# Optimization experiments

Hardware: AMD Instinct MI355X
Metric: run time of the kernel (lower is better)

Reference implementation:

```python
import jax, jax.numpy as jnp
import numpy as np

B, S, D, K = 16384, 32, 64, 3
LN_EPS = 1e-6
ENT_EPS = 1e-10
SUM_EPS = 1e-6


def _layernorm(x, g, b):
    m = x.mean(-1, keepdims=True)
    v = ((x - m) ** 2).mean(-1, keepdims=True)
    return (x - m) * jax.lax.rsqrt(v + LN_EPS) * g + b


def setup_inputs() -> dict:
    key = jax.random.key(0)
    ks = jax.random.split(key, 8)
    return {
        "gw_r": jax.random.normal(ks[0], (B, D), jnp.float32),
        "gw_i": jax.random.normal(ks[1], (B, D), jnp.float32),
        "mem_r": jax.random.normal(ks[2], (B, S, D), jnp.float32),
        "mem_i": jax.random.normal(ks[3], (B, S, D), jnp.float32),
        # gate_net: Linear(2D -> 1); stored as [in, out]
        "Wg": jax.random.normal(ks[4], (2 * D, 1), jnp.float32) * 0.05,
        "bg": jnp.zeros((1,), jnp.float32),
        # address_net: Linear(2D -> slots)
        "Wa": jax.random.normal(ks[5], (2 * D, S), jnp.float32) * 0.05,
        "ba": jnp.zeros((S,), jnp.float32),
        # StableComplexNorm affine params
        "g_r": jnp.ones((D,), jnp.float32),
        "b_r": jnp.zeros((D,), jnp.float32),
        "g_i": jnp.ones((D,), jnp.float32),
        "b_i": jnp.zeros((D,), jnp.float32),
    }


def reference(gw_r, gw_i, mem_r, mem_i, Wg, bg, Wa, ba, g_r, b_r, g_i, b_i):
    # --- Read: cosine-style similarity Re(conj(mem) * q).sum(-1) ---
    sim = jnp.einsum("bsd,bd->bs", mem_r, gw_r) + jnp.einsum("bsd,bd->bs", mem_i, gw_i)
    sim = sim - jax.lax.stop_gradient(sim.max(-1, keepdims=True))
    attn = jax.nn.softmax(sim, axis=-1)  # [B, S]
    read_r = jnp.einsum("bs,bsd->bd", attn, mem_r)
    read_i = jnp.einsum("bs,bsd->bd", attn, mem_i)

    # --- Write gate + address ---
    flat = jnp.concatenate([gw_r, gw_i], axis=-1)  # [B, 2D]
    write_gate = jax.nn.sigmoid(flat @ Wg + bg)  # [B, 1]
    logits = flat @ Wa + ba  # [B, S]
    logits = logits - jax.lax.stop_gradient(logits.max(-1, keepdims=True))
    ww = jax.nn.softmax(logits, axis=-1)  # [B, S]
    slot_entropy = -(ww * jnp.log(ww + ENT_EPS)).sum(-1).mean()

    # --- Top-k sparse scatter write weights ---
    top_vals, top_idx = jax.lax.top_k(ww, K)  # [B, K]
    sparse = jnp.zeros_like(ww).at[jnp.arange(B)[:, None], top_idx].set(top_vals)
    sparse = sparse / (sparse.sum(-1, keepdims=True) + SUM_EPS)

    # effective_update: [B, S, 1]
    eu = write_gate[:, None, :] * sparse[..., None]
    next_r = (1.0 - eu) * mem_r + eu * gw_r[:, None, :]
    next_i = (1.0 - eu) * mem_i + eu * gw_i[:, None, :]

    # --- Dual LayerNorm on real/imag independently ---
    next_r = _layernorm(next_r, g_r, b_r)
    next_i = _layernorm(next_i, g_i, b_i)

    return (read_r, read_i, next_r, next_i, slot_entropy)
```

## Files before the change

kernel.cpp:

```cpp
#include <hip/hip_runtime.h>
#include <cstddef>

constexpr int Bn = 16384;
constexpr int Sn = 32;
constexpr int Dn = 64;

__device__ __forceinline__ float red16(float v) {
    v += __shfl_xor(v, 1);
    v += __shfl_xor(v, 2);
    v += __shfl_xor(v, 4);
    v += __shfl_xor(v, 8);
    return v;
}

__device__ __forceinline__ float4 red_groups(float4 v) {
    v.x += __shfl_xor(v.x, 16); v.y += __shfl_xor(v.y, 16);
    v.z += __shfl_xor(v.z, 16); v.w += __shfl_xor(v.w, 16);
    v.x += __shfl_xor(v.x, 32); v.y += __shfl_xor(v.y, 32);
    v.z += __shfl_xor(v.z, 32); v.w += __shfl_xor(v.w, 32);
    return v;
}

__global__ __launch_bounds__(256, 4) void amem_fwd(
    const float* __restrict__ gw_r, const float* __restrict__ gw_i,
    const float* __restrict__ mem_r, const float* __restrict__ mem_i,
    const float* __restrict__ Wg,   const float* __restrict__ bg,
    const float* __restrict__ Wa,   const float* __restrict__ ba,
    const float* __restrict__ g_r,  const float* __restrict__ b_r,
    const float* __restrict__ g_i,  const float* __restrict__ b_i,
    float* __restrict__ o_read_r, float* __restrict__ o_read_i,
    float* __restrict__ o_next_r, float* __restrict__ o_next_i,
    float* __restrict__ ws_ent)
{
    __shared__ float sWa[4096];
    __shared__ float lflat[4][128];

    const int tid  = threadIdx.x;
    const int wave = tid >> 6;
    const int l    = tid & 63;
    const int b    = blockIdx.x * 4 + wave;
    const int g    = l >> 4;
    const int q    = l & 15;

    const float4* mr4 = (const float4*)mem_r + (size_t)b * 512;
    const float4* mi4 = (const float4*)mem_i + (size_t)b * 512;
    float4 m_r[8], m_i[8];
#pragma unroll
    for (int k = 0; k < 8; ++k) {
        m_r[k] = mr4[k * 64 + l];
        m_i[k] = mi4[k * 64 + l];
    }
    const float4 q4r = ((const float4*)gw_r)[b * 16 + q];
    const float4 q4i = ((const float4*)gw_i)[b * 16 + q];

    {
        const float4* Wa4 = (const float4*)Wa;
        float4* sWa4 = (float4*)sWa;
#pragma unroll
        for (int j = 0; j < 4; ++j) sWa4[tid + 256 * j] = Wa4[tid + 256 * j];
    }
    if (g == 0)      *(float4*)&lflat[wave][q * 4]      = q4r;
    else if (g == 1) *(float4*)&lflat[wave][64 + q * 4] = q4i;
    __syncthreads();

    float sims[8];
#pragma unroll
    for (int k = 0; k < 8; ++k) {
        float p = m_r[k].x * q4r.x + m_r[k].y * q4r.y + m_r[k].z * q4r.z + m_r[k].w * q4r.w
                + m_i[k].x * q4i.x + m_i[k].y * q4i.y + m_i[k].z * q4i.z + m_i[k].w * q4i.w;
        sims[k] = red16(p);
    }
    float mx = sims[0];
#pragma unroll
    for (int k = 1; k < 8; ++k) mx = fmaxf(mx, sims[k]);
    mx = fmaxf(mx, __shfl_xor(mx, 16));
    mx = fmaxf(mx, __shfl_xor(mx, 32));
    float attn[8];
    float asum = 0.f;
#pragma unroll
    for (int k = 0; k < 8; ++k) { attn[k] = __expf(sims[k] - mx); asum += attn[k]; }
    asum += __shfl_xor(asum, 16);
    asum += __shfl_xor(asum, 32);
    const float ainv = 1.0f / asum;

    float4 rr = {0.f, 0.f, 0.f, 0.f}, ri = {0.f, 0.f, 0.f, 0.f};
#pragma unroll
    for (int k = 0; k < 8; ++k) {
        const float a = attn[k] * ainv;
        rr.x = fmaf(a, m_r[k].x, rr.x); rr.y = fmaf(a, m_r[k].y, rr.y);
        rr.z = fmaf(a, m_r[k].z, rr.z); rr.w = fmaf(a, m_r[k].w, rr.w);
        ri.x = fmaf(a, m_i[k].x, ri.x); ri.y = fmaf(a, m_i[k].y, ri.y);
        ri.z = fmaf(a, m_i[k].z, ri.z); ri.w = fmaf(a, m_i[k].w, ri.w);
    }
    rr = red_groups(rr);
    ri = red_groups(ri);
    if (g == 0) {
        ((float4*)o_read_r)[b * 16 + q] = rr;
        ((float4*)o_read_i)[b * 16 + q] = ri;
    }

    const float4 wg0 = ((const float4*)Wg)[q];
    const float4 wg1 = ((const float4*)Wg)[16 + q];
    float wp = q4r.x * wg0.x + q4r.y * wg0.y + q4r.z * wg0.z + q4r.w * wg0.w
             + q4i.x * wg1.x + q4i.y * wg1.y + q4i.z * wg1.z + q4i.w * wg1.w;
    wp = red16(wp);
    const float wgate = 1.0f / (1.0f + __expf(-(wp + bg[0])));

    const int sl = l & 31;
    const int h  = l >> 5;
    const float* WaL = sWa + h * 2048;
    const float4* lf4 = (const float4*)&lflat[wave][h * 64];
    float a0 = 0.f, a1 = 0.f, a2 = 0.f, a3 = 0.f;
#pragma unroll
    for (int jj = 0; jj < 16; ++jj) {
        const float4 f = lf4[jj];
        const int r0 = jj * 4;
        a0 = fmaf(f.x, WaL[(r0 + 0) * 32 + sl], a0);
        a1 = fmaf(f.y, WaL[(r0 + 1) * 32 + sl], a1);
        a2 = fmaf(f.z, WaL[(r0 + 2) * 32 + sl], a2);
        a3 = fmaf(f.w, WaL[(r0 + 3) * 32 + sl], a3);
    }
    float acc = (a0 + a1) + (a2 + a3);
    acc += __shfl_xor(acc, 32);
    acc += ba[sl];

    float lm = acc;
    lm = fmaxf(lm, __shfl_xor(lm, 1));
    lm = fmaxf(lm, __shfl_xor(lm, 2));
    lm = fmaxf(lm, __shfl_xor(lm, 4));
    lm = fmaxf(lm, __shfl_xor(lm, 8));
    lm = fmaxf(lm, __shfl_xor(lm, 16));
    const float we = __expf(acc - lm);
    float wsum = we;
    wsum += __shfl_xor(wsum, 1);
    wsum += __shfl_xor(wsum, 2);
    wsum += __shfl_xor(wsum, 4);
    wsum += __shfl_xor(wsum, 8);
    wsum += __shfl_xor(wsum, 16);
    const float ww = we / wsum;

    float et = ww * __logf(ww + 1e-10f);
    et += __shfl_xor(et, 1);
    et += __shfl_xor(et, 2);
    et += __shfl_xor(et, 4);
    et += __shfl_xor(et, 8);
    et += __shfl_xor(et, 16);
    if (l == 0) ws_ent[b] = -et;

    float lv = ww;
    float v1, v2, v3;
    int   i1, i2, i3;
#pragma unroll
    for (int pass = 0; pass < 3; ++pass) {
        float bv = lv;
        int   bi = sl;
#pragma unroll
        for (int d = 1; d <= 16; d <<= 1) {
            const float ov = __shfl_xor(bv, d);
            const int   oi = __shfl_xor(bi, d);
            if (ov > bv || (ov == bv && oi < bi)) { bv = ov; bi = oi; }
        }
        if (pass == 0) { v1 = bv; i1 = bi; }
        else if (pass == 1) { v2 = bv; i2 = bi; }
        else { v3 = bv; i3 = bi; }
        if (sl == bi) lv = -1.f;
    }
    const float inv_ssum = 1.0f / (v1 + v2 + v3 + 1e-6f);

    const float4 gr  = ((const float4*)g_r)[q];
    const float4 br  = ((const float4*)b_r)[q];
    const float4 gi  = ((const float4*)g_i)[q];
    const float4 bi4 = ((const float4*)b_i)[q];
    float4* onr = (float4*)o_next_r + (size_t)b * 512;
    float4* oni = (float4*)o_next_i + (size_t)b * 512;

#pragma unroll
    for (int k = 0; k < 8; ++k) {
        const int s = k * 4 + g;
        const float sp = (s == i1) ? v1 : (s == i2) ? v2 : (s == i3) ? v3 : 0.f;
        const float eu = wgate * sp * inv_ssum;
        const float om = 1.f - eu;

        float4 xr, xi;
        xr.x = om * m_r[k].x + eu * q4r.x;
        xr.y = om * m_r[k].y + eu * q4r.y;
        xr.z = om * m_r[k].z + eu * q4r.z;
        xr.w = om * m_r[k].w + eu * q4r.w;
        xi.x = om * m_i[k].x + eu * q4i.x;
        xi.y = om * m_i[k].y + eu * q4i.y;
        xi.z = om * m_i[k].z + eu * q4i.z;
        xi.w = om * m_i[k].w + eu * q4i.w;

        float sr = (xr.x + xr.y) + (xr.z + xr.w);
        float si = (xi.x + xi.y) + (xi.z + xi.w);
        float qr = xr.x * xr.x; qr = fmaf(xr.y, xr.y, qr); qr = fmaf(xr.z, xr.z, qr); qr = fmaf(xr.w, xr.w, qr);
        float qi = xi.x * xi.x; qi = fmaf(xi.y, xi.y, qi); qi = fmaf(xi.z, xi.z, qi); qi = fmaf(xi.w, xi.w, qi);

#pragma unroll
        for (int d2 = 1; d2 <= 8; d2 <<= 1) {
            sr += __shfl_xor(sr, d2);
            si += __shfl_xor(si, d2);
            qr += __shfl_xor(qr, d2);
            qi += __shfl_xor(qi, d2);
        }

        const float mr_ = sr * (1.f / 64.f);
        const float mi_ = si * (1.f / 64.f);
        const float vr  = qr * (1.f / 64.f) - mr_ * mr_;
        const float vi  = qi * (1.f / 64.f) - mi_ * mi_;
        const float ar  = rsqrtf(vr + 1e-6f);
        const float ai  = rsqrtf(vi + 1e-6f);
        const float cr  = -mr_ * ar;
        const float ci  = -mi_ * ai;

        float4 yr, yi;
        yr.x = fmaf(fmaf(xr.x, ar, cr), gr.x, br.x);
        yr.y = fmaf(fmaf(xr.y, ar, cr), gr.y, br.y);
        yr.z = fmaf(fmaf(xr.z, ar, cr), gr.z, br.z);
        yr.w = fmaf(fmaf(xr.w, ar, cr), gr.w, br.w);
        yi.x = fmaf(fmaf(xi.x, ai, ci), gi.x, bi4.x);
        yi.y = fmaf(fmaf(xi.y, ai, ci), gi.y, bi4.y);
        yi.z = fmaf(fmaf(xi.z, ai, ci), gi.z, bi4.z);
        yi.w = fmaf(fmaf(xi.w, ai, ci), gi.w, bi4.w);
        onr[k * 64 + l] = yr;
        oni[k * 64 + l] = yi;
    }
}

__global__ __launch_bounds__(1024) void ent_reduce(const float* __restrict__ ws_ent,
                                                   float* __restrict__ o_ent)
{
    __shared__ float red[1024];
    const int t = threadIdx.x;
    float s = 0.f;
    for (int i = t; i < Bn; i += 1024) s += ws_ent[i];
    red[t] = s;
    __syncthreads();
    for (int st = 512; st > 0; st >>= 1) {
        if (t < st) red[t] += red[t + st];
        __syncthreads();
    }
    if (t == 0) o_ent[0] = red[0] * (1.0f / (float)Bn);
}

extern "C" void kernel_launch(void* const* d_in, const int* in_sizes, int n_in,
                              void* d_out, int out_size, void* d_ws, size_t ws_size,
                              hipStream_t stream)
{
    const float* gw_r  = (const float*)d_in[0];
    const float* gw_i  = (const float*)d_in[1];
    const float* mem_r = (const float*)d_in[2];
    const float* mem_i = (const float*)d_in[3];
    const float* Wg    = (const float*)d_in[4];
    const float* bg    = (const float*)d_in[5];
    const float* Wa    = (const float*)d_in[6];
    const float* ba    = (const float*)d_in[7];
    const float* g_r   = (const float*)d_in[8];
    const float* b_r   = (const float*)d_in[9];
    const float* g_i   = (const float*)d_in[10];
    const float* b_i   = (const float*)d_in[11];

    float* out = (float*)d_out;
    const size_t nBD  = (size_t)Bn * Dn;
    const size_t nBSD = (size_t)Bn * Sn * Dn;
    float* o_read_r = out;
    float* o_read_i = out + nBD;
    float* o_next_r = out + 2 * nBD;
    float* o_next_i = out + 2 * nBD + nBSD;
    float* o_ent    = out + 2 * nBD + 2 * nBSD;

    float* ws_ent = (float*)d_ws;

    amem_fwd<<<Bn / 4, 256, 0, stream>>>(
        gw_r, gw_i, mem_r, mem_i, Wg, bg, Wa, ba, g_r, b_r, g_i, b_i,
        o_read_r, o_read_i, o_next_r, o_next_i, ws_ent);
    ent_reduce<<<1, 1024, 0, stream>>>(ws_ent, o_ent);
}
```

Before: 122.3 us.

## Stream memory rows twice instead of holding them in registers, raise occupancy

The main kernel no longer keeps all 64 floats of mem_r/mem_i per lane in registers across the whole computation. It reads the memory once to compute similarities and softmax. It then re-reads mem_r and mem_i in two separate passes that fuse the attention read-out with the gated update and LayerNorm. Launch bounds are raised from 4 to 8 blocks per SM to exploit the lower register pressure. The cost is a second read of the 64 MB memory tensors, which likely hits L2/MALL only partially and could increase DRAM traffic for this bandwidth-bound kernel.

Result: slower. 319.8 us (+161.6%).

```diff
diff --git a/kernel.cpp b/kernel.cpp
--- a/kernel.cpp
+++ b/kernel.cpp
@@ -21,7 +21,7 @@
     return v;
 }
 
-__global__ __launch_bounds__(256, 4) void amem_fwd(
+__global__ __launch_bounds__(256, 8) void amem_fwd(
     const float* __restrict__ gw_r, const float* __restrict__ gw_i,
     const float* __restrict__ mem_r, const float* __restrict__ mem_i,
     const float* __restrict__ Wg,   const float* __restrict__ bg,
@@ -42,14 +42,6 @@
     const int g    = l >> 4;
     const int q    = l & 15;
 
-    const float4* mr4 = (const float4*)mem_r + (size_t)b * 512;
-    const float4* mi4 = (const float4*)mem_i + (size_t)b * 512;
-    float4 m_r[8], m_i[8];
-#pragma unroll
-    for (int k = 0; k < 8; ++k) {
-        m_r[k] = mr4[k * 64 + l];
-        m_i[k] = mi4[k * 64 + l];
-    }
     const float4 q4r = ((const float4*)gw_r)[b * 16 + q];
     const float4 q4i = ((const float4*)gw_i)[b * 16 + q];
 
@@ -62,42 +54,6 @@
     if (g == 0)      *(float4*)&lflat[wave][q * 4]      = q4r;
     else if (g == 1) *(float4*)&lflat[wave][64 + q * 4] = q4i;
     __syncthreads();
-
-    float sims[8];
-#pragma unroll
-    for (int k = 0; k < 8; ++k) {
-        float p = m_r[k].x * q4r.x + m_r[k].y * q4r.y + m_r[k].z * q4r.z + m_r[k].w * q4r.w
-                + m_i[k].x * q4i.x + m_i[k].y * q4i.y + m_i[k].z * q4i.z + m_i[k].w * q4i.w;
-        sims[k] = red16(p);
-    }
-    float mx = sims[0];
-#pragma unroll
-    for (int k = 1; k < 8; ++k) mx = fmaxf(mx, sims[k]);
-    mx = fmaxf(mx, __shfl_xor(mx, 16));
-    mx = fmaxf(mx, __shfl_xor(mx, 32));
-    float attn[8];
-    float asum = 0.f;
-#pragma unroll
-    for (int k = 0; k < 8; ++k) { attn[k] = __expf(sims[k] - mx); asum += attn[k]; }
-    asum += __shfl_xor(asum, 16);
-    asum += __shfl_xor(asum, 32);
-    const float ainv = 1.0f / asum;
-
-    float4 rr = {0.f, 0.f, 0.f, 0.f}, ri = {0.f, 0.f, 0.f, 0.f};
-#pragma unroll
-    for (int k = 0; k < 8; ++k) {
-        const float a = attn[k] * ainv;
-        rr.x = fmaf(a, m_r[k].x, rr.x); rr.y = fmaf(a, m_r[k].y, rr.y);
-        rr.z = fmaf(a, m_r[k].z, rr.z); rr.w = fmaf(a, m_r[k].w, rr.w);
-        ri.x = fmaf(a, m_i[k].x, ri.x); ri.y = fmaf(a, m_i[k].y, ri.y);
-        ri.z = fmaf(a, m_i[k].z, ri.z); ri.w = fmaf(a, m_i[k].w, ri.w);
-    }
-    rr = red_groups(rr);
-    ri = red_groups(ri);
-    if (g == 0) {
-        ((float4*)o_read_r)[b * 16 + q] = rr;
-        ((float4*)o_read_i)[b * 16 + q] = ri;
-    }
 
     const float4 wg0 = ((const float4*)Wg)[q];
     const float4 wg1 = ((const float4*)Wg)[16 + q];
@@ -167,63 +123,120 @@
     }
     const float inv_ssum = 1.0f / (v1 + v2 + v3 + 1e-6f);
 
-    const float4 gr  = ((const float4*)g_r)[q];
-    const float4 br  = ((const float4*)b_r)[q];
-    const float4 gi  = ((const float4*)g_i)[q];
-    const float4 bi4 = ((const float4*)b_i)[q];
-    float4* onr = (float4*)o_next_r + (size_t)b * 512;
-    float4* oni = (float4*)o_next_i + (size_t)b * 512;
-
+    const float4* mr4 = (const float4*)mem_r + (size_t)b * 512;
+    const float4* mi4 = (const float4*)mem_i + (size_t)b * 512;
+    float sims[8];
 #pragma unroll
     for (int k = 0; k < 8; ++k) {
-        const int s = k * 4 + g;
-        const float sp = (s == i1) ? v1 : (s == i2) ? v2 : (s == i3) ? v3 : 0.f;
-        const float eu = wgate * sp * inv_ssum;
-        const float om = 1.f - eu;
-
-        float4 xr, xi;
-        xr.x = om * m_r[k].x + eu * q4r.x;
-        xr.y = om * m_r[k].y + eu * q4r.y;
-        xr.z = om * m_r[k].z + eu * q4r.z;
-        xr.w = om * m_r[k].w + eu * q4r.w;
-        xi.x = om * m_i[k].x + eu * q4i.x;
-        xi.y = om * m_i[k].y + eu * q4i.y;
-        xi.z = om * m_i[k].z + eu * q4i.z;
-        xi.w = om * m_i[k].w + eu * q4i.w;
-
-        float sr = (xr.x + xr.y) + (xr.z + xr.w);
-        float si = (xi.x + xi.y) + (xi.z + xi.w);
-        float qr = xr.x * xr.x; qr = fmaf(xr.y, xr.y, qr); qr = fmaf(xr.z, xr.z, qr); qr = fmaf(xr.w, xr.w, qr);
-        float qi = xi.x * xi.x; qi = fmaf(xi.y, xi.y, qi); qi = fmaf(xi.z, xi.z, qi); qi = fmaf(xi.w, xi.w, qi);
-
-#pragma unroll
-        for (int d2 = 1; d2 <= 8; d2 <<= 1) {
-            sr += __shfl_xor(sr, d2);
-            si += __shfl_xor(si, d2);
-            qr += __shfl_xor(qr, d2);
-            qi += __shfl_xor(qi, d2);
+        const float4 a = mr4[k * 64 + l];
+        const float4 c = mi4[k * 64 + l];
+        float p = a.x * q4r.x + a.y * q4r.y + a.z * q4r.z + a.w * q4r.w
+                + c.x * q4i.x + c.y * q4i.y + c.z * q4i.z + c.w * q4i.w;
+        sims[k] = red16(p);
+    }
+    float mx = sims[0];
+#pragma unroll
+    for (int k = 1; k < 8; ++k) mx = fmaxf(mx, sims[k]);
+    mx = fmaxf(mx, __shfl_xor(mx, 16));
+    mx = fmaxf(mx, __shfl_xor(mx, 32));
+    float attn[8];
+    float asum = 0.f;
+#pragma unroll
+    for (int k = 0; k < 8; ++k) { attn[k] = __expf(sims[k] - mx); asum += attn[k]; }
+    asum += __shfl_xor(asum, 16);
+    asum += __shfl_xor(asum, 32);
+    const float ainv = 1.0f / asum;
+#pragma unroll
+    for (int k = 0; k < 8; ++k) attn[k] *= ainv;
+
+    {
+        const float4 gr = ((const float4*)g_r)[q];
+        const float4 br = ((const float4*)b_r)[q];
+        float4* onr = (float4*)o_next_r + (size_t)b * 512;
+        float4 rr = {0.f, 0.f, 0.f, 0.f};
+#pragma unroll
+        for (int k = 0; k < 8; ++k) {
+            const float4 m = mr4[k * 64 + l];
+            rr.x = fmaf(attn[k], m.x, rr.x); rr.y = fmaf(attn[k], m.y, rr.y);
+            rr.z = fmaf(attn[k], m.z, rr.z); rr.w = fmaf(attn[k], m.w, rr.w);
+
+            const int s = k * 4 + g;
+            const float sp = (s == i1) ? v1 : (s == i2) ? v2 : (s == i3) ? v3 : 0.f;
+            const float eu = wgate * sp * inv_ssum;
+            const float om = 1.f - eu;
+
+            float4 x;
+            x.x = om * m.x + eu * q4r.x;
+            x.y = om * m.y + eu * q4r.y;
+            x.z = om * m.z + eu * q4r.z;
+            x.w = om * m.w + eu * q4r.w;
+
+            float sr = (x.x + x.y) + (x.z + x.w);
+            float qr = x.x * x.x; qr = fmaf(x.y, x.y, qr); qr = fmaf(x.z, x.z, qr); qr = fmaf(x.w, x.w, qr);
+#pragma unroll
+            for (int d2 = 1; d2 <= 8; d2 <<= 1) {
+                sr += __shfl_xor(sr, d2);
+                qr += __shfl_xor(qr, d2);
+            }
+            const float mean = sr * (1.f / 64.f);
+            const float var  = qr * (1.f / 64.f) - mean * mean;
+            const float rs   = rsqrtf(var + 1e-6f);
+            const float c0   = -mean * rs;
+
+            float4 y;
+            y.x = fmaf(fmaf(x.x, rs, c0), gr.x, br.x);
+            y.y = fmaf(fmaf(x.y, rs, c0), gr.y, br.y);
+            y.z = fmaf(fmaf(x.z, rs, c0), gr.z, br.z);
+            y.w = fmaf(fmaf(x.w, rs, c0), gr.w, br.w);
+            onr[k * 64 + l] = y;
         }
-
-        const float mr_ = sr * (1.f / 64.f);
-        const float mi_ = si * (1.f / 64.f);
-        const float vr  = qr * (1.f / 64.f) - mr_ * mr_;
-        const float vi  = qi * (1.f / 64.f) - mi_ * mi_;
-        const float ar  = rsqrtf(vr + 1e-6f);
-        const float ai  = rsqrtf(vi + 1e-6f);
-        const float cr  = -mr_ * ar;
-        const float ci  = -mi_ * ai;
-
-        float4 yr, yi;
-        yr.x = fmaf(fmaf(xr.x, ar, cr), gr.x, br.x);
-        yr.y = fmaf(fmaf(xr.y, ar, cr), gr.y, br.y);
-        yr.z = fmaf(fmaf(xr.z, ar, cr), gr.z, br.z);
-        yr.w = fmaf(fmaf(xr.w, ar, cr), gr.w, br.w);
-        yi.x = fmaf(fmaf(xi.x, ai, ci), gi.x, bi4.x);
-        yi.y = fmaf(fmaf(xi.y, ai, ci), gi.y, bi4.y);
-        yi.z = fmaf(fmaf(xi.z, ai, ci), gi.z, bi4.z);
-        yi.w = fmaf(fmaf(xi.w, ai, ci), gi.w, bi4.w);
-        onr[k * 64 + l] = yr;
-        oni[k * 64 + l] = yi;
+        rr = red_groups(rr);
+        if (g == 0) ((float4*)o_read_r)[b * 16 + q] = rr;
+    }
+
+    {
+        const float4 gi  = ((const float4*)g_i)[q];
+        const float4 bi4 = ((const float4*)b_i)[q];
+        float4* oni = (float4*)o_next_i + (size_t)b * 512;
+        float4 ri = {0.f, 0.f, 0.f, 0.f};
+#pragma unroll
+        for (int k = 0; k < 8; ++k) {
+            const float4 m = mi4[k * 64 + l];
+            ri.x = fmaf(attn[k], m.x, ri.x); ri.y = fmaf(attn[k], m.y, ri.y);
+            ri.z = fmaf(attn[k], m.z, ri.z); ri.w = fmaf(attn[k], m.w, ri.w);
+
+            const int s = k * 4 + g;
+            const float sp = (s == i1) ? v1 : (s == i2) ? v2 : (s == i3) ? v3 : 0.f;
+            const float eu = wgate * sp * inv_ssum;
+            const float om = 1.f - eu;
+
+            float4 x;
+            x.x = om * m.x + eu * q4i.x;
+            x.y = om * m.y + eu * q4i.y;
+            x.z = om * m.z + eu * q4i.z;
+            x.w = om * m.w + eu * q4i.w;
+
+            float si = (x.x + x.y) + (x.z + x.w);
+            float qi = x.x * x.x; qi = fmaf(x.y, x.y, qi); qi = fmaf(x.z, x.z, qi); qi = fmaf(x.w, x.w, qi);
+#pragma unroll
+            for (int d2 = 1; d2 <= 8; d2 <<= 1) {
+                si += __shfl_xor(si, d2);
+                qi += __shfl_xor(qi, d2);
+            }
+            const float mean = si * (1.f / 64.f);
+            const float var  = qi * (1.f / 64.f) - mean * mean;
+            const float rs   = rsqrtf(var + 1e-6f);
+            const float c0   = -mean * rs;
+
+            float4 y;
+            y.x = fmaf(fmaf(x.x, rs, c0), gi.x, bi4.x);
+            y.y = fmaf(fmaf(x.y, rs, c0), gi.y, bi4.y);
+            y.z = fmaf(fmaf(x.z, rs, c0), gi.z, bi4.z);
+            y.w = fmaf(fmaf(x.w, rs, c0), gi.w, bi4.w);
+            oni[k * 64 + l] = y;
+        }
+        ri = red_groups(ri);
+        if (g == 0) ((float4*)o_read_i)[b * 16 + q] = ri;
     }
 }
 
```

## Split write-address computation into separate kernel and use DPP reductions

Applied to the files above, without the earlier changes.

Moves the gate, address softmax, entropy and top-3 selection into a lightweight pre-kernel that writes per-row metadata, so the main memory-bound kernel no longer stages Wa into LDS, synchronises, or runs the address matmul. The main kernel reads the metadata, fuses the read-accumulation into the LayerNorm loop, and replaces 16-lane shuffle reductions with DPP row operations. This adds a kernel launch and a small workspace round trip in exchange for lighter LDS use and fewer instructions in the bandwidth-bound path.

Result: slower. 264.8 us (+116.6%).

```diff
diff --git a/kernel.cpp b/kernel.cpp
--- a/kernel.cpp
+++ b/kernel.cpp
@@ -4,6 +4,25 @@
 constexpr int Bn = 16384;
 constexpr int Sn = 32;
 constexpr int Dn = 64;
+
+__device__ __forceinline__ float dpp_add(float v, const int ctrl) {
+    int t;
+    switch (ctrl) {
+        case 0xB1:  t = __builtin_amdgcn_update_dpp(0, __builtin_bit_cast(int, v), 0xB1, 0xF, 0xF, true); break;
+        case 0x4E:  t = __builtin_amdgcn_update_dpp(0, __builtin_bit_cast(int, v), 0x4E, 0xF, 0xF, true); break;
+        case 0x141: t = __builtin_amdgcn_update_dpp(0, __builtin_bit_cast(int, v), 0x141, 0xF, 0xF, true); break;
+        default:    t = __builtin_amdgcn_update_dpp(0, __builtin_bit_cast(int, v), 0x140, 0xF, 0xF, true); break;
+    }
+    return v + __builtin_bit_cast(float, t);
+}
+
+__device__ __forceinline__ float red16_dpp(float v) {
+    v = dpp_add(v, 0xB1);
+    v = dpp_add(v, 0x4E);
+    v = dpp_add(v, 0x141);
+    v = dpp_add(v, 0x140);
+    return v;
+}
 
 __device__ __forceinline__ float red16(float v) {
     v += __shfl_xor(v, 1);
@@ -13,28 +32,125 @@
     return v;
 }
 
-__device__ __forceinline__ float4 red_groups(float4 v) {
-    v.x += __shfl_xor(v.x, 16); v.y += __shfl_xor(v.y, 16);
-    v.z += __shfl_xor(v.z, 16); v.w += __shfl_xor(v.w, 16);
-    v.x += __shfl_xor(v.x, 32); v.y += __shfl_xor(v.y, 32);
-    v.z += __shfl_xor(v.z, 32); v.w += __shfl_xor(v.w, 32);
-    return v;
-}
-
-__global__ __launch_bounds__(256, 4) void amem_fwd(
+__global__ __launch_bounds__(256, 8) void amem_meta(
     const float* __restrict__ gw_r, const float* __restrict__ gw_i,
-    const float* __restrict__ mem_r, const float* __restrict__ mem_i,
     const float* __restrict__ Wg,   const float* __restrict__ bg,
     const float* __restrict__ Wa,   const float* __restrict__ ba,
-    const float* __restrict__ g_r,  const float* __restrict__ b_r,
-    const float* __restrict__ g_i,  const float* __restrict__ b_i,
-    float* __restrict__ o_read_r, float* __restrict__ o_read_i,
-    float* __restrict__ o_next_r, float* __restrict__ o_next_i,
-    float* __restrict__ ws_ent)
+    float* __restrict__ meta, float* __restrict__ ws_ent)
 {
     __shared__ float sWa[4096];
     __shared__ float lflat[4][128];
 
+    const int tid  = threadIdx.x;
+    const int wave = tid >> 6;
+    const int l    = tid & 63;
+    const int g    = l >> 4;
+    const int q    = l & 15;
+    const int sl   = l & 31;
+    const int h    = l >> 5;
+
+    {
+        const float4* Wa4 = (const float4*)Wa;
+        float4* sWa4 = (float4*)sWa;
+#pragma unroll
+        for (int j = 0; j < 4; ++j) sWa4[tid + 256 * j] = Wa4[tid + 256 * j];
+    }
+    __syncthreads();
+
+    const float bg0 = bg[0];
+    const float ba_sl = ba[sl];
+    const float4 wg0 = ((const float4*)Wg)[q];
+    const float4 wg1 = ((const float4*)Wg)[16 + q];
+
+    for (int r = 0; r < 4; ++r) {
+        const int b = blockIdx.x * 16 + wave * 4 + r;
+        const float4 q4r = ((const float4*)gw_r)[b * 16 + q];
+        const float4 q4i = ((const float4*)gw_i)[b * 16 + q];
+
+        if (g == 0)      *(float4*)&lflat[wave][q * 4]      = q4r;
+        else if (g == 1) *(float4*)&lflat[wave][64 + q * 4] = q4i;
+
+        float wp = q4r.x * wg0.x + q4r.y * wg0.y + q4r.z * wg0.z + q4r.w * wg0.w
+                 + q4i.x * wg1.x + q4i.y * wg1.y + q4i.z * wg1.z + q4i.w * wg1.w;
+        wp = red16(wp);
+        const float wgate = 1.0f / (1.0f + __expf(-(wp + bg0)));
+
+        const float* WaL = sWa + h * 2048;
+        const float4* lf4 = (const float4*)&lflat[wave][h * 64];
+        float a0 = 0.f, a1 = 0.f, a2 = 0.f, a3 = 0.f;
+#pragma unroll
+        for (int jj = 0; jj < 16; ++jj) {
+            const float4 f = lf4[jj];
+            const int r0 = jj * 4;
+            a0 = fmaf(f.x, WaL[(r0 + 0) * 32 + sl], a0);
+            a1 = fmaf(f.y, WaL[(r0 + 1) * 32 + sl], a1);
+            a2 = fmaf(f.z, WaL[(r0 + 2) * 32 + sl], a2);
+            a3 = fmaf(f.w, WaL[(r0 + 3) * 32 + sl], a3);
+        }
+        float acc = (a0 + a1) + (a2 + a3);
+        acc += __shfl_xor(acc, 32);
+        acc += ba_sl;
+
+        float lm = acc;
+        lm = fmaxf(lm, __shfl_xor(lm, 1));
+        lm = fmaxf(lm, __shfl_xor(lm, 2));
+        lm = fmaxf(lm, __shfl_xor(lm, 4));
+        lm = fmaxf(lm, __shfl_xor(lm, 8));
+        lm = fmaxf(lm, __shfl_xor(lm, 16));
+        const float we = __expf(acc - lm);
+        float wsum = we;
+        wsum += __shfl_xor(wsum, 1);
+        wsum += __shfl_xor(wsum, 2);
+        wsum += __shfl_xor(wsum, 4);
+        wsum += __shfl_xor(wsum, 8);
+        wsum += __shfl_xor(wsum, 16);
+        const float ww = we / wsum;
+
+        float et = ww * __logf(ww + 1e-10f);
+        et += __shfl_xor(et, 1);
+        et += __shfl_xor(et, 2);
+        et += __shfl_xor(et, 4);
+        et += __shfl_xor(et, 8);
+        et += __shfl_xor(et, 16);
+
+        float lv = ww;
+        float v1, v2, v3;
+        int   i1, i2, i3;
+#pragma unroll
+        for (int pass = 0; pass < 3; ++pass) {
+            float bv = lv;
+            int   bi = sl;
+#pragma unroll
+            for (int d = 1; d <= 16; d <<= 1) {
+                const float ov = __shfl_xor(bv, d);
+                const int   oi = __shfl_xor(bi, d);
+                if (ov > bv || (ov == bv && oi < bi)) { bv = ov; bi = oi; }
+            }
+            if (pass == 0) { v1 = bv; i1 = bi; }
+            else if (pass == 1) { v2 = bv; i2 = bi; }
+            else { v3 = bv; i3 = bi; }
+            if (sl == bi) lv = -1.f;
+        }
+
+        if (l == 0) {
+            ws_ent[b] = -et;
+            float4 m0 = {v1, v2, v3, wgate};
+            float4 m1 = {(float)i1, (float)i2, (float)i3, 0.f};
+            ((float4*)meta)[b * 2]     = m0;
+            ((float4*)meta)[b * 2 + 1] = m1;
+        }
+    }
+}
+
+__global__ __launch_bounds__(256, 4) void amem_main(
+    const float* __restrict__ gw_r, const float* __restrict__ gw_i,
+    const float* __restrict__ mem_r, const float* __restrict__ mem_i,
+    const float* __restrict__ g_r,  const float* __restrict__ b_r,
+    const float* __restrict__ g_i,  const float* __restrict__ b_i,
+    const float* __restrict__ meta,
+    float* __restrict__ o_read_r, float* __restrict__ o_read_i,
+    float* __restrict__ o_next_r, float* __restrict__ o_next_i)
+{
     const int tid  = threadIdx.x;
     const int wave = tid >> 6;
     const int l    = tid & 63;
@@ -53,22 +169,23 @@
     const float4 q4r = ((const float4*)gw_r)[b * 16 + q];
     const float4 q4i = ((const float4*)gw_i)[b * 16 + q];
 
-    {
-        const float4* Wa4 = (const float4*)Wa;
-        float4* sWa4 = (float4*)sWa;
-#pragma unroll
-        for (int j = 0; j < 4; ++j) sWa4[tid + 256 * j] = Wa4[tid + 256 * j];
-    }
-    if (g == 0)      *(float4*)&lflat[wave][q * 4]      = q4r;
-    else if (g == 1) *(float4*)&lflat[wave][64 + q * 4] = q4i;
-    __syncthreads();
+    const float4 m0 = ((const float4*)meta)[b * 2];
+    const float4 m1 = ((const float4*)meta)[b * 2 + 1];
+    const float v1 = m0.x, v2 = m0.y, v3 = m0.z, wgate = m0.w;
+    const int   i1 = (int)m1.x, i2 = (int)m1.y, i3 = (int)m1.z;
+    const float inv_ssum = 1.0f / (v1 + v2 + v3 + 1e-6f);
+
+    const float4 gr  = ((const float4*)g_r)[q];
+    const float4 br  = ((const float4*)b_r)[q];
+    const float4 gi  = ((const float4*)g_i)[q];
+    const float4 bi4 = ((const float4*)b_i)[q];
 
     float sims[8];
 #pragma unroll
     for (int k = 0; k < 8; ++k) {
         float p = m_r[k].x * q4r.x + m_r[k].y * q4r.y + m_r[k].z * q4r.z + m_r[k].w * q4r.w
                 + m_i[k].x * q4i.x + m_i[k].y * q4i.y + m_i[k].z * q4i.z + m_i[k].w * q4i.w;
-        sims[k] = red16(p);
+        sims[k] = red16_dpp(p);
     }
     float mx = sims[0];
 #pragma unroll
@@ -82,100 +199,20 @@
     asum += __shfl_xor(asum, 16);
     asum += __shfl_xor(asum, 32);
     const float ainv = 1.0f / asum;
-
-    float4 rr = {0.f, 0.f, 0.f, 0.f}, ri = {0.f, 0.f, 0.f, 0.f};
-#pragma unroll
-    for (int k = 0; k < 8; ++k) {
-        const float a = attn[k] * ainv;
-        rr.x = fmaf(a, m_r[k].x, rr.x); rr.y = fmaf(a, m_r[k].y, rr.y);
-        rr.z = fmaf(a, m_r[k].z, rr.z); rr.w = fmaf(a, m_r[k].w, rr.w);
-        ri.x = fmaf(a, m_i[k].x, ri.x); ri.y = fmaf(a, m_i[k].y, ri.y);
-        ri.z = fmaf(a, m_i[k].z, ri.z); ri.w = fmaf(a, m_i[k].w, ri.w);
-    }
-    rr = red_groups(rr);
-    ri = red_groups(ri);
-    if (g == 0) {
-        ((float4*)o_read_r)[b * 16 + q] = rr;
-        ((float4*)o_read_i)[b * 16 + q] = ri;
-    }
-
-    const float4 wg0 = ((const float4*)Wg)[q];
-    const float4 wg1 = ((const float4*)Wg)[16 + q];
-    float wp = q4r.x * wg0.x + q4r.y * wg0.y + q4r.z * wg0.z + q4r.w * wg0.w
-             + q4i.x * wg1.x + q4i.y * wg1.y + q4i.z * wg1.z + q4i.w * wg1.w;
-    wp = red16(wp);
-    const float wgate = 1.0f / (1.0f + __expf(-(wp + bg[0])));
-
-    const int sl = l & 31;
-    const int h  = l >> 5;
-    const float* WaL = sWa + h * 2048;
-    const float4* lf4 = (const float4*)&lflat[wave][h * 64];
-    float a0 = 0.f, a1 = 0.f, a2 = 0.f, a3 = 0.f;
-#pragma unroll
-    for (int jj = 0; jj < 16; ++jj) {
-        const float4 f = lf4[jj];
-        const int r0 = jj * 4;
-        a0 = fmaf(f.x, WaL[(r0 + 0) * 32 + sl], a0);
-        a1 = fmaf(f.y, WaL[(r0 + 1) * 32 + sl], a1);
-        a2 = fmaf(f.z, WaL[(r0 + 2) * 32 + sl], a2);
-        a3 = fmaf(f.w, WaL[(r0 + 3) * 32 + sl], a3);
-    }
-    float acc = (a0 + a1) + (a2 + a3);
-    acc += __shfl_xor(acc, 32);
-    acc += ba[sl];
-
-    float lm = acc;
-    lm = fmaxf(lm, __shfl_xor(lm, 1));
-    lm = fmaxf(lm, __shfl_xor(lm, 2));
-    lm = fmaxf(lm, __shfl_xor(lm, 4));
-    lm = fmaxf(lm, __shfl_xor(lm, 8));
-    lm = fmaxf(lm, __shfl_xor(lm, 16));
-    const float we = __expf(acc - lm);
-    float wsum = we;
-    wsum += __shfl_xor(wsum, 1);
-    wsum += __shfl_xor(wsum, 2);
-    wsum += __shfl_xor(wsum, 4);
-    wsum += __shfl_xor(wsum, 8);
-    wsum += __shfl_xor(wsum, 16);
-    const float ww = we / wsum;
-
-    float et = ww * __logf(ww + 1e-10f);
-    et += __shfl_xor(et, 1);
-    et += __shfl_xor(et, 2);
-    et += __shfl_xor(et, 4);
-    et += __shfl_xor(et, 8);
-    et += __shfl_xor(et, 16);
-    if (l == 0) ws_ent[b] = -et;
-
-    float lv = ww;
-    float v1, v2, v3;
-    int   i1, i2, i3;
-#pragma unroll
-    for (int pass = 0; pass < 3; ++pass) {
-        float bv = lv;
-        int   bi = sl;
-#pragma unroll
-        for (int d = 1; d <= 16; d <<= 1) {
-            const float ov = __shfl_xor(bv, d);
-            const int   oi = __shfl_xor(bi, d);
-            if (ov > bv || (ov == bv && oi < bi)) { bv = ov; bi = oi; }
-        }
-        if (pass == 0) { v1 = bv; i1 = bi; }
-        else if (pass == 1) { v2 = bv; i2 = bi; }
-        else { v3 = bv; i3 = bi; }
-        if (sl == bi) lv = -1.f;
-    }
-    const float inv_ssum = 1.0f / (v1 + v2 + v3 + 1e-6f);
-
-    const float4 gr  = ((const float4*)g_r)[q];
-    const float4 br  = ((const float4*)b_r)[q];
-    const float4 gi  = ((const float4*)g_i)[q];
-    const float4 bi4 = ((const float4*)b_i)[q];
+#pragma unroll
+    for (int k = 0; k < 8; ++k) attn[k] *= ainv;
+
     float4* onr = (float4*)o_next_r + (size_t)b * 512;
     float4* oni = (float4*)o_next_i + (size_t)b * 512;
+    float4 rr = {0.f, 0.f, 0.f, 0.f}, ri = {0.f, 0.f, 0.f, 0.f};
 
 #pragma unroll
     for (int k = 0; k < 8; ++k) {
+        rr.x = fmaf(attn[k], m_r[k].x, rr.x); rr.y = fmaf(attn[k], m_r[k].y, rr.y);
+        rr.z = fmaf(attn[k], m_r[k].z, rr.z); rr.w = fmaf(attn[k], m_r[k].w, rr.w);
+        ri.x = fmaf(attn[k], m_i[k].x, ri.x); ri.y = fmaf(attn[k], m_i[k].y, ri.y);
+        ri.z = fmaf(attn[k], m_i[k].z, ri.z); ri.w = fmaf(attn[k], m_i[k].w, ri.w);
+
         const int s = k * 4 + g;
         const float sp = (s == i1) ? v1 : (s == i2) ? v2 : (s == i3) ? v3 : 0.f;
         const float eu = wgate * sp * inv_ssum;
@@ -196,13 +233,10 @@
         float qr = xr.x * xr.x; qr = fmaf(xr.y, xr.y, qr); qr = fmaf(xr.z, xr.z, qr); qr = fmaf(xr.w, xr.w, qr);
         float qi = xi.x * xi.x; qi = fmaf(xi.y, xi.y, qi); qi = fmaf(xi.z, xi.z, qi); qi = fmaf(xi.w, xi.w, qi);
 
-#pragma unroll
-        for (int d2 = 1; d2 <= 8; d2 <<= 1) {
-            sr += __shfl_xor(sr, d2);
-            si += __shfl_xor(si, d2);
-            qr += __shfl_xor(qr, d2);
-            qi += __shfl_xor(qi, d2);
-        }
+        sr = red16_dpp(sr);
+        si = red16_dpp(si);
+        qr = red16_dpp(qr);
+        qi = red16_dpp(qi);
 
         const float mr_ = sr * (1.f / 64.f);
         const float mi_ = si * (1.f / 64.f);
@@ -224,6 +258,19 @@
         yi.w = fmaf(fmaf(xi.w, ai, ci), gi.w, bi4.w);
         onr[k * 64 + l] = yr;
         oni[k * 64 + l] = yi;
+    }
+
+    rr.x += __shfl_xor(rr.x, 16); rr.y += __shfl_xor(rr.y, 16);
+    rr.z += __shfl_xor(rr.z, 16); rr.w += __shfl_xor(rr.w, 16);
+    rr.x += __shfl_xor(rr.x, 32); rr.y += __shfl_xor(rr.y, 32);
+    rr.z += __shfl_xor(rr.z, 32); rr.w += __shfl_xor(rr.w, 32);
+    ri.x += __shfl_xor(ri.x, 16); ri.y += __shfl_xor(ri.y, 16);
+    ri.z += __shfl_xor(ri.z, 16); ri.w += __shfl_xor(ri.w, 16);
+    ri.x += __shfl_xor(ri.x, 32); ri.y += __shfl_xor(ri.y, 32);
+    ri.z += __shfl_xor(ri.z, 32); ri.w += __shfl_xor(ri.w, 32);
+    if (g == 0) {
+        ((float4*)o_read_r)[b * 16 + q] = rr;
+        ((float4*)o_read_i)[b * 16 + q] = ri;
     }
 }
 
@@ -270,9 +317,11 @@
     float* o_ent    = out + 2 * nBD + 2 * nBSD;
 
     float* ws_ent = (float*)d_ws;
-
-    amem_fwd<<<Bn / 4, 256, 0, stream>>>(
-        gw_r, gw_i, mem_r, mem_i, Wg, bg, Wa, ba, g_r, b_r, g_i, b_i,
-        o_read_r, o_read_i, o_next_r, o_next_i, ws_ent);
+    float* meta   = (float*)d_ws + Bn;
+
+    amem_meta<<<Bn / 16, 256, 0, stream>>>(gw_r, gw_i, Wg, bg, Wa, ba, meta, ws_ent);
+    amem_main<<<Bn / 4, 256, 0, stream>>>(gw_r, gw_i, mem_r, mem_i,
+                                          g_r, b_r, g_i, b_i, meta,
+                                          o_read_r, o_read_i, o_next_r, o_next_i);
     ent_reduce<<<1, 1024, 0, stream>>>(ws_ent, o_ent);
 }
```
